# Optimization experiments

Measured on AMD Instinct MI355X. Metric: run time of the kernel, lower is better.

The kernel has to match this reference:

```python
import jax, jax.numpy as jnp
import numpy as np

NEG_SLOPE = 0.2

def gat_layer(x, src, dst, W, b, a_src, a_dst, heads, out_dim, concat):
    N = x.shape[0]
    h = (x @ W).reshape(N, heads, out_dim)            # [N,H,D]
    s_src = jnp.sum(h * a_src, axis=-1)               # [N,H]
    s_dst = jnp.sum(h * a_dst, axis=-1)               # [N,H]
    e = jax.nn.leaky_relu(s_src[src] + s_dst[dst], NEG_SLOPE)  # [E,H]
    # segment softmax over destination nodes (self-loops guarantee nonempty segments)
    m = jax.ops.segment_max(e, dst, num_segments=N)
    e = jnp.exp(e - m[dst])
    denom = jax.ops.segment_sum(e, dst, num_segments=N)
    alpha = e / denom[dst]                            # [E,H]
    msg = h[src] * alpha[:, :, None]                  # [E,H,D]
    out = jax.ops.segment_sum(msg, dst, num_segments=N)  # [N,H,D]
    if concat:
        out = out.reshape(N, heads * out_dim)
    else:
        out = out.mean(axis=1)
    return out + b

def setup_inputs() -> dict:
    key = jax.random.key(0)
    ks = jax.random.split(key, 16)
    N, E = 50000, 1600000
    IN, HID, OUT, H = 128, 256, 32, 4
    D = HID // H
    def glorot(k, shape):
        fan = shape[0] + shape[-1]
        return jax.random.uniform(k, shape, jnp.float32, -1.0, 1.0) * np.sqrt(6.0 / fan)
    x = jax.random.normal(ks[0], (N, IN), jnp.float32)
    edge_index = jax.random.randint(ks[1], (2, E), 0, N, jnp.int32)
    return {
        "x": x, "edge_index": edge_index,
        "W0": glorot(ks[2], (IN, H * D)), "b0": jnp.zeros((H * D,), jnp.float32),
        "asrc0": glorot(ks[3], (H, D)), "adst0": glorot(ks[4], (H, D)),
        "W1": glorot(ks[5], (HID, H * D)), "b1": jnp.zeros((H * D,), jnp.float32),
        "asrc1": glorot(ks[6], (H, D)), "adst1": glorot(ks[7], (H, D)),
        "W2": glorot(ks[8], (HID, 1 * OUT)), "b2": jnp.zeros((OUT,), jnp.float32),
        "asrc2": glorot(ks[9], (1, OUT)), "adst2": glorot(ks[10], (1, OUT)),
    }

def reference(x, edge_index, W0, b0, asrc0, adst0, W1, b1, asrc1, adst1, W2, b2, asrc2, adst2):
    N = x.shape[0]
    # add self-loops (PyG GATConv default)
    loop = jnp.arange(N, dtype=edge_index.dtype)
    src = jnp.concatenate([edge_index[0], loop])
    dst = jnp.concatenate([edge_index[1], loop])
    h = gat_layer(x, src, dst, W0, b0, asrc0, adst0, heads=4, out_dim=64, concat=True)
    h = jax.nn.elu(h)
    h = gat_layer(h, src, dst, W1, b1, asrc1, adst1, heads=4, out_dim=64, concat=True)
    h = jax.nn.elu(h)
    h = gat_layer(h, src, dst, W2, b2, asrc2, adst2, heads=1, out_dim=32, concat=False)
    return jax.nn.log_softmax(h, axis=1)
```

## Files before the change

### kernel.cpp

```cpp
#include <hip/hip_runtime.h>
#include <hip/hip_bf16.h>
#include <math.h>

#define IN_DIM 128
#define HID    256
#define OUTD   32
#define HEADS  4
#define NB_SH  7
#define BUCKET_CAP 6144
#define NCHUNK_BLKS 256
#define DCAP   96

typedef __attribute__((ext_vector_type(8))) short s8v;
typedef __attribute__((ext_vector_type(4))) float f4v;

__device__ inline unsigned short f2bf(float f) {
    union { __hip_bfloat16 b; unsigned short u; } cv;
    cv.b = __float2bfloat16(f);
    return cv.u;
}


__global__ __launch_bounds__(256) void csr_hist(const int* __restrict__ ei,
                                                int* __restrict__ H,
                                                int E, int N, int NB, int per_blk) {
    __shared__ int hist[512];
    int t = threadIdx.x;
    for (int i = t; i < NB; i += 256) hist[i] = 0;
    __syncthreads();
    int lo = blockIdx.x * per_blk;
    int hi = min(lo + per_blk, E + N);
    for (int e = lo + t; e < hi; e += 256) {
        int dst = (e < E) ? ei[E + e] : (e - E);
        atomicAdd(&hist[dst >> NB_SH], 1);
    }
    __syncthreads();
    for (int i = t; i < NB; i += 256) H[blockIdx.x * NB + i] = hist[i];
}

__global__ __launch_bounds__(256) void csr_colscan(int* __restrict__ H,
                                                   int* __restrict__ total, int NB) {
    int b = blockIdx.x, t = threadIdx.x;
    int v = H[t * NB + b];
    __shared__ int s[256];
    s[t] = v;
    __syncthreads();
    for (int o = 1; o < 256; o <<= 1) {
        int x = (t >= o) ? s[t - o] : 0;
        __syncthreads();
        s[t] += x;
        __syncthreads();
    }
    H[t * NB + b] = s[t] - v;
    if (t == 255) total[b] = s[255];
}

__global__ void csr_basescan(const int* __restrict__ total, int* __restrict__ base, int NB) {
    __shared__ int s[512];
    int t = threadIdx.x;
    int v = (t < NB) ? total[t] : 0;
    s[t] = v;
    __syncthreads();
    for (int o = 1; o < 512; o <<= 1) {
        int x = (t >= o) ? s[t - o] : 0;
        __syncthreads();
        s[t] += x;
        __syncthreads();
    }
    if (t < NB) base[t] = s[t] - v;
    if (t == NB - 1) base[NB] = s[t];
}

__global__ __launch_bounds__(256) void csr_partition(const int* __restrict__ ei,
                                                     const int* __restrict__ H,
                                                     const int* __restrict__ base,
                                                     int* __restrict__ ebuf,
                                                     int E, int N, int per_blk, int NB) {
    __shared__ int cur[512];
    int t = threadIdx.x;
    for (int i = t; i < NB; i += 256) cur[i] = base[i] + H[blockIdx.x * NB + i];
    __syncthreads();
    int lo = blockIdx.x * per_blk;
    int hi = min(lo + per_blk, E + N);
    for (int e = lo + t; e < hi; e += 256) {
        int src = (e < E) ? ei[e] : (e - E);
        int dst = (e < E) ? ei[E + e] : (e - E);
        int pos = atomicAdd(&cur[dst >> NB_SH], 1);
        ebuf[pos] = src | ((dst & 127) << 16);
    }
}

__global__ __launch_bounds__(256) void csr_sort(const int* __restrict__ ebuf,
                                                const int* __restrict__ base,
                                                int* __restrict__ col,
                                                int* __restrict__ rp, int N, int NB) {
    int b = blockIdx.x, t = threadIdx.x;
    int lo = base[b], hi = base[b + 1];
    int nbase = b << NB_SH;
    __shared__ int c_[128], sc[128], cur[128];
    __shared__ int loc[BUCKET_CAP];
    if (t < 128) c_[t] = 0;
    __syncthreads();
    for (int k = lo + t; k < hi; k += 256) atomicAdd(&c_[(ebuf[k] >> 16) & 127], 1);
    __syncthreads();
    if (t < 128) sc[t] = c_[t];
    __syncthreads();
    for (int o = 1; o < 128; o <<= 1) {
        int x = 0;
        if (t < 128 && t >= o) x = sc[t - o];
        __syncthreads();
        if (t < 128) sc[t] += x;
        __syncthreads();
    }
    if (t < 128) {
        int excl = sc[t] - c_[t];
        cur[t] = excl;
        int node = nbase + t;
        if (node < N) rp[node] = lo + excl;
    }
    if (b == NB - 1 && t == 0) rp[N] = hi;
    __syncthreads();
    for (int k = lo + t; k < hi; k += 256) {
        int e = ebuf[k];
        int p = atomicAdd(&cur[(e >> 16) & 127], 1);
        if (p < BUCKET_CAP) loc[p] = e & 0xFFFF;
    }
    __syncthreads();
    int m = min(hi - lo, BUCKET_CAP);
    for (int k = t; k < m; k += 256) col[lo + k] = loc[k];
}


__global__ __launch_bounds__(256) void prep_w(const float* __restrict__ W,
                                              unsigned short* __restrict__ Wt_h,
                                              unsigned short* __restrict__ Wt_l,
                                              int K, int N) {
    int idx = blockIdx.x * 256 + threadIdx.x;
    if (idx >= K * N) return;
    int n = idx / K, k = idx % K;
    float x = W[(size_t)k * N + n];
    unsigned short h = f2bf(x);
    float hf = __uint_as_float((unsigned)h << 16);
    Wt_h[idx] = h;
    Wt_l[idx] = f2bf(x - hf);
}

__global__ __launch_bounds__(256) void prep_x(const float* __restrict__ X,
                                              unsigned short* __restrict__ Xh,
                                              unsigned short* __restrict__ Xl,
                                              int total8) {
    int idx = blockIdx.x * 256 + threadIdx.x;
    if (idx >= total8) return;
    size_t b = (size_t)idx * 8;
    float4 v0 = *(const float4*)(X + b);
    float4 v1 = *(const float4*)(X + b + 4);
    float x[8] = {v0.x, v0.y, v0.z, v0.w, v1.x, v1.y, v1.z, v1.w};
    union { unsigned short s[8]; uint4 q; } h, l;
#pragma unroll
    for (int j = 0; j < 8; j++) {
        h.s[j] = f2bf(x[j]);
        l.s[j] = f2bf(x[j] - __uint_as_float((unsigned)h.s[j] << 16));
    }
    *(uint4*)(Xh + b) = h.q;
    *(uint4*)(Xl + b) = l.q;
}


template <int BN>
__global__ __launch_bounds__(256, 2) void gemm_mfma(const unsigned short* __restrict__ Ah,
                                                    const unsigned short* __restrict__ Al,
                                                    const unsigned short* __restrict__ Wt_h,
                                                    const unsigned short* __restrict__ Wt_l,
                                                    unsigned short* __restrict__ Cb,
                                                    const float* __restrict__ asrc,
                                                    const float* __restrict__ adst,
                                                    float* __restrict__ ssrcO,
                                                    float* __restrict__ sdstO,
                                                    int M, int K, int Nst, int Hn) {
    constexpr int WROWS = (BN == 128) ? 64 : 32;
    constexpr int WCOLS = (BN == 128) ? 64 : 32;
    constexpr int MI = WROWS / 16, NJ = WCOLS / 16;
    __shared__ unsigned short As_h[128][64], As_l[128][64];
    __shared__ unsigned short Bs_h[BN][64], Bs_l[BN][64];
    int tid = threadIdx.x;
    int lane = tid & 63, w = tid >> 6;
    int wm, wn;
    if (BN == 128) { wm = w & 1; wn = w >> 1; } else { wm = w; wn = 0; }
    int row0 = blockIdx.x * 128, col0 = blockIdx.y * BN;

    f4v acc[MI][NJ];
#pragma unroll
    for (int i = 0; i < MI; i++)
#pragma unroll
        for (int j = 0; j < NJ; j++) acc[i][j] = (f4v)(0.f);

    for (int k0 = 0; k0 < K; k0 += 64) {
#pragma unroll
        for (int i = 0; i < 4; i++) {
            int cidx = tid + i * 256;
            int r = cidx >> 3, ch = cidx & 7;
            int grow = row0 + r;
            uint4 vh = make_uint4(0, 0, 0, 0), vl = make_uint4(0, 0, 0, 0);
            if (grow < M) {
                size_t g = (size_t)grow * K + k0 + ch * 8;
                vh = *(const uint4*)(Ah + g);
                vl = *(const uint4*)(Al + g);
            }
            int chs = ch ^ (r & 7);
            *(uint4*)&As_h[r][chs * 8] = vh;
            *(uint4*)&As_l[r][chs * 8] = vl;
        }
#pragma unroll
        for (int i = 0; i < BN * 8 / 256; i++) {
            int cidx = tid + i * 256;
            int n = cidx >> 3, ch = cidx & 7;
            int chs = ch ^ (n & 7);
            size_t g = (size_t)(col0 + n) * K + k0 + ch * 8;
            *(uint4*)&Bs_h[n][chs * 8] = *(const uint4*)(Wt_h + g);
            *(uint4*)&Bs_l[n][chs * 8] = *(const uint4*)(Wt_l + g);
        }
        __syncthreads();
#pragma unroll
        for (int ks = 0; ks < 2; ks++) {
            s8v ah[MI], al[MI], bh[NJ], bl[NJ];
            int kc = ks * 4 + (lane >> 4);
            int lr = lane & 15;
#pragma unroll
            for (int i = 0; i < MI; i++) {
                int r = wm * WROWS + i * 16 + lr;
                ah[i] = *(const s8v*)&As_h[r][(kc ^ (r & 7)) * 8];
                al[i] = *(const s8v*)&As_l[r][(kc ^ (r & 7)) * 8];
            }
#pragma unroll
            for (int j = 0; j < NJ; j++) {
                int n = wn * WCOLS + j * 16 + lr;
                bh[j] = *(const s8v*)&Bs_h[n][(kc ^ (n & 7)) * 8];
                bl[j] = *(const s8v*)&Bs_l[n][(kc ^ (n & 7)) * 8];
            }
#pragma unroll
            for (int i = 0; i < MI; i++)
#pragma unroll
                for (int j = 0; j < NJ; j++) {
                    acc[i][j] = __builtin_amdgcn_mfma_f32_16x16x32_bf16(ah[i], bh[j], acc[i][j], 0, 0, 0);
                    acc[i][j] = __builtin_amdgcn_mfma_f32_16x16x32_bf16(ah[i], bl[j], acc[i][j], 0, 0, 0);
                    acc[i][j] = __builtin_amdgcn_mfma_f32_16x16x32_bf16(al[i], bh[j], acc[i][j], 0, 0, 0);
                }
        }
        __syncthreads();
    }
    int lr = lane & 15, lg = lane >> 4;
#pragma unroll
    for (int i = 0; i < MI; i++)
#pragma unroll
        for (int j = 0; j < NJ; j++) {
            int gcol = col0 + wn * WCOLS + j * 16 + lr;
#pragma unroll
            for (int rr = 0; rr < 4; rr++) {
                int grow = row0 + wm * WROWS + i * 16 + lg * 4 + rr;
                if (grow < M) Cb[(size_t)grow * Nst + gcol] = f2bf(acc[i][j][rr]);
            }
        }
    int hd = (BN == 128) ? (blockIdx.y * 2 + wn) : 0;
    float as_[NJ], ad_[NJ];
#pragma unroll
    for (int j = 0; j < NJ; j++) {
        int gcol = col0 + wn * WCOLS + j * 16 + lr;
        as_[j] = asrc[gcol];
        ad_[j] = adst[gcol];
    }
#pragma unroll
    for (int i = 0; i < MI; i++)
#pragma unroll
        for (int rr = 0; rr < 4; rr++) {
            float ps = 0.f, pd = 0.f;
#pragma unroll
            for (int j = 0; j < NJ; j++) {
                ps += acc[i][j][rr] * as_[j];
                pd += acc[i][j][rr] * ad_[j];
            }
#pragma unroll
            for (int off = 1; off < 16; off <<= 1) {
                ps += __shfl_xor(ps, off);
                pd += __shfl_xor(pd, off);
            }
            int grow = row0 + wm * WROWS + i * 16 + lg * 4 + rr;
            if (lr == 0 && grow < M) {
                ssrcO[(size_t)grow * Hn + hd] = ps;
                sdstO[(size_t)grow * Hn + hd] = pd;
            }
        }
}


__global__ __launch_bounds__(256) void gat_fused256(const unsigned short* __restrict__ hb,
                                                    const float* __restrict__ ssrc,
                                                    const float* __restrict__ sdst,
                                                    const int* __restrict__ rp,
                                                    const int* __restrict__ col,
                                                    const float* __restrict__ bias,
                                                    unsigned short* __restrict__ outH,
                                                    unsigned short* __restrict__ outL, int N) {
    __shared__ float als[4][DCAP * 4];
    int wv = threadIdx.x >> 6, lane = threadIdx.x & 63;
    int n = blockIdx.x * 4 + wv;
    if (n >= N) return;
    int k0 = __builtin_amdgcn_readfirstlane(rp[n]);
    int k1 = __builtin_amdgcn_readfirstlane(rp[n + 1]);
    int deg = k1 - k0;

    int h1 = lane & 3, slot = lane >> 2;
    float sd1 = sdst[(size_t)n * 4 + h1];
    float m = -1e30f, l = 0.f;
    for (int k = k0 + slot; k < k1; k += 16) {
        int s = col[k];
        float e = ssrc[(size_t)s * 4 + h1] + sd1;
        e = (e > 0.f) ? e : 0.2f * e;
        float mn = fmaxf(m, e);
        l = l * __expf(m - mn) + __expf(e - mn);
        m = mn;
    }
#pragma unroll
    for (int off = 4; off < 64; off <<= 1) {
        float m2 = __shfl_xor(m, off), l2 = __shfl_xor(l, off);
        float mn = fmaxf(m, m2);
        l = l * __expf(m - mn) + l2 * __expf(m2 - mn);
        m = mn;
    }
    float invl = 1.f / l;
    bool fast = (deg <= DCAP);
    if (fast) {
        for (int k = k0 + slot; k < k1; k += 16) {
            int s = col[k];
            float e = ssrc[(size_t)s * 4 + h1] + sd1;
            e = (e > 0.f) ? e : 0.2f * e;
            als[wv][(k - k0) * 4 + h1] = __expf(e - m) * invl;
        }
    }

    int eo = lane >> 4;
    int cl = (lane & 15) * 8;
#pragma unroll
    for (int half = 0; half < 2; half++) {
        int c = half * 128 + cl;
        int head = c >> 6;
        float acc[8];
#pragma unroll
        for (int j = 0; j < 8; j++) acc[j] = 0.f;
        if (fast) {
            for (int k = k0; k < k1; k += 8) {
                int ka = k + eo, kb = k + 4 + eo;
                bool va = ka < k1, vb = kb < k1;
                int sa = col[va ? ka : k0], sb = col[vb ? kb : k0];
                int ia = va ? (ka - k0) : 0, ib = vb ? (kb - k0) : 0;
                float aa = va ? als[wv][ia * 4 + head] : 0.f;
                float ab = vb ? als[wv][ib * 4 + head] : 0.f;
                uint4 ha = *(const uint4*)(hb + (size_t)sa * 256 + c);
                uint4 hc = *(const uint4*)(hb + (size_t)sb * 256 + c);
                const unsigned* pa = (const unsigned*)&ha;
                const unsigned* pb = (const unsigned*)&hc;
#pragma unroll
                for (int q = 0; q < 4; q++) {
                    acc[2 * q]     += aa * __uint_as_float(pa[q] << 16)
                                    + ab * __uint_as_float(pb[q] << 16);
                    acc[2 * q + 1] += aa * __uint_as_float(pa[q] & 0xffff0000u)
                                    + ab * __uint_as_float(pb[q] & 0xffff0000u);
                }
            }
        } else {
            float mh = __shfl(m, head);
            float ivh = __shfl(invl, head);
            float sdh = __shfl(sd1, head);
            for (int k = k0; k < k1; k += 8) {
                int ka = k + eo, kb = k + 4 + eo;
                bool va = ka < k1, vb = kb < k1;
                int sa = col[va ? ka : k0], sb = col[vb ? kb : k0];
                float ea = ssrc[(size_t)sa * 4 + head] + sdh;
                ea = (ea > 0.f) ? ea : 0.2f * ea;
                float aa = va ? __expf(ea - mh) * ivh : 0.f;
                float eb = ssrc[(size_t)sb * 4 + head] + sdh;
                eb = (eb > 0.f) ? eb : 0.2f * eb;
                float ab = vb ? __expf(eb - mh) * ivh : 0.f;
                uint4 ha = *(const uint4*)(hb + (size_t)sa * 256 + c);
                uint4 hc = *(const uint4*)(hb + (size_t)sb * 256 + c);
                const unsigned* pa = (const unsigned*)&ha;
                const unsigned* pb = (const unsigned*)&hc;
#pragma unroll
                for (int q = 0; q < 4; q++) {
                    acc[2 * q]     += aa * __uint_as_float(pa[q] << 16)
                                    + ab * __uint_as_float(pb[q] << 16);
                    acc[2 * q + 1] += aa * __uint_as_float(pa[q] & 0xffff0000u)
                                    + ab * __uint_as_float(pb[q] & 0xffff0000u);
                }
            }
        }
#pragma unroll
        for (int off = 16; off < 64; off <<= 1)
#pragma unroll
            for (int j = 0; j < 8; j++) acc[j] += __shfl_xor(acc[j], off);
        if (eo == 0) {
            union { unsigned short s[8]; uint4 q; } ph, pl;
#pragma unroll
            for (int j = 0; j < 8; j++) {
                float v = acc[j] + bias[c + j];
                v = (v > 0.f) ? v : expm1f(v);
                ph.s[j] = f2bf(v);
                pl.s[j] = f2bf(v - __uint_as_float((unsigned)ph.s[j] << 16));
            }
            *(uint4*)(outH + (size_t)n * 256 + c) = ph.q;
            *(uint4*)(outL + (size_t)n * 256 + c) = pl.q;
        }
    }
}


__global__ __launch_bounds__(256) void gat_fused32(const unsigned short* __restrict__ hb,
                                                   const float* __restrict__ ssrc,
                                                   const float* __restrict__ sdst,
                                                   const int* __restrict__ rp,
                                                   const int* __restrict__ col,
                                                   const float* __restrict__ bias,
                                                   float* __restrict__ outF, int N) {
    const int TPE = 4, EPW = 16;
    int wv = threadIdx.x >> 6, lane = threadIdx.x & 63;
    int n = blockIdx.x * 4 + wv;
    if (n >= N) return;
    int k0 = __builtin_amdgcn_readfirstlane(rp[n]);
    int k1 = __builtin_amdgcn_readfirstlane(rp[n + 1]);

    float sd1 = sdst[n];
    float m = -1e30f, l = 0.f;
    for (int k = k0 + lane; k < k1; k += 64) {
        int s = col[k];
        float e = ssrc[s] + sd1;
        e = (e > 0.f) ? e : 0.2f * e;
        float mn = fmaxf(m, e);
        l = l * __expf(m - mn) + __expf(e - mn);
        m = mn;
    }
#pragma unroll
    for (int off = 1; off < 64; off <<= 1) {
        float m2 = __shfl_xor(m, off), l2 = __shfl_xor(l, off);
        float mn = fmaxf(m, m2);
        l = l * __expf(m - mn) + l2 * __expf(m2 - mn);
        m = mn;
    }
    float invl = 1.f / l;

    int eo = lane / TPE;
    int c = (lane % TPE) * 8;
    float acc[8];
#pragma unroll
    for (int j = 0; j < 8; j++) acc[j] = 0.f;
    for (int k = k0; k < k1; k += 2 * EPW) {
        int ka = k + eo, kb = k + EPW + eo;
        bool va = ka < k1, vb = kb < k1;
        int sa = col[va ? ka : k0], sb = col[vb ? kb : k0];
        float ea = ssrc[sa] + sd1;
        ea = (ea > 0.f) ? ea : 0.2f * ea;
        float aa = va ? __expf(ea - m) * invl : 0.f;
        float eb = ssrc[sb] + sd1;
        eb = (eb > 0.f) ? eb : 0.2f * eb;
        float ab = vb ? __expf(eb - m) * invl : 0.f;
        uint4 ha = *(const uint4*)(hb + (size_t)sa * 32 + c);
        uint4 hc = *(const uint4*)(hb + (size_t)sb * 32 + c);
        const unsigned* pa = (const unsigned*)&ha;
        const unsigned* pb = (const unsigned*)&hc;
#pragma unroll
        for (int q = 0; q < 4; q++) {
            acc[2 * q]     += aa * __uint_as_float(pa[q] << 16)
                            + ab * __uint_as_float(pb[q] << 16);
            acc[2 * q + 1] += aa * __uint_as_float(pa[q] & 0xffff0000u)
                            + ab * __uint_as_float(pb[q] & 0xffff0000u);
        }
    }
#pragma unroll
    for (int off = TPE; off < 64; off <<= 1)
#pragma unroll
        for (int j = 0; j < 8; j++) acc[j] += __shfl_xor(acc[j], off);

    float o[8];
#pragma unroll
    for (int j = 0; j < 8; j++) o[j] = acc[j] + bias[c + j];
    float mx = o[0];
#pragma unroll
    for (int j = 1; j < 8; j++) mx = fmaxf(mx, o[j]);
#pragma unroll
    for (int off = 1; off < TPE; off <<= 1) mx = fmaxf(mx, __shfl_xor(mx, off));
    float sm = 0.f;
#pragma unroll
    for (int j = 0; j < 8; j++) sm += __expf(o[j] - mx);
#pragma unroll
    for (int off = 1; off < TPE; off <<= 1) sm += __shfl_xor(sm, off);
    float lg = logf(sm) + mx;
    if (eo != 0) return;
    float4* op = (float4*)(outF + (size_t)n * 32 + c);
    op[0] = make_float4(o[0] - lg, o[1] - lg, o[2] - lg, o[3] - lg);
    op[1] = make_float4(o[4] - lg, o[5] - lg, o[6] - lg, o[7] - lg);
}


extern "C" void kernel_launch(void* const* d_in, const int* in_sizes, int n_in,
                              void* d_out, int out_size, void* d_ws, size_t ws_size,
                              hipStream_t stream) {
    const float* x   = (const float*)d_in[0];
    const int*   ei  = (const int*)d_in[1];
    const float* W0  = (const float*)d_in[2];
    const float* b0  = (const float*)d_in[3];
    const float* as0 = (const float*)d_in[4];
    const float* ad0 = (const float*)d_in[5];
    const float* W1  = (const float*)d_in[6];
    const float* b1  = (const float*)d_in[7];
    const float* as1 = (const float*)d_in[8];
    const float* ad1 = (const float*)d_in[9];
    const float* W2  = (const float*)d_in[10];
    const float* b2  = (const float*)d_in[11];
    const float* as2 = (const float*)d_in[12];
    const float* ad2 = (const float*)d_in[13];

    int N = in_sizes[0] / IN_DIM;
    int E = in_sizes[1] / 2;
    int Et = E + N;
    int NB = (N + 127) >> NB_SH;

    char* w = (char*)d_ws;
    size_t off = 0;
    auto alloc = [&](size_t bytes) -> void* {
        void* p = w + off;
        off = (off + bytes + 255) & ~(size_t)255;
        return p;
    };
    unsigned short* Qh    = (unsigned short*)alloc((size_t)N * HID * 2);
    unsigned short* Ql    = (unsigned short*)alloc((size_t)N * HID * 2);
    unsigned short* Ab    = (unsigned short*)alloc((size_t)N * HID * 2);
    unsigned short* xh    = (unsigned short*)alloc((size_t)N * IN_DIM * 2);
    unsigned short* xl    = (unsigned short*)alloc((size_t)N * IN_DIM * 2);
    float*          ssrc  = (float*)alloc((size_t)N * HEADS * 4);
    float*          sdst  = (float*)alloc((size_t)N * HEADS * 4);
    int*            rp    = (int*)alloc((size_t)(N + 1) * 4);
    int*            col   = (int*)alloc((size_t)Et * 4);
    int*            H     = (int*)alloc((size_t)NCHUNK_BLKS * NB * 4);
    int*            total = (int*)alloc((size_t)(NB + 1) * 4);
    int*            base  = (int*)alloc((size_t)(NB + 1) * 4);
    int*            ebuf  = (int*)alloc((size_t)Et * 4);
    unsigned short* Wt0h  = (unsigned short*)alloc((size_t)IN_DIM * HID * 2);
    unsigned short* Wt0l  = (unsigned short*)alloc((size_t)IN_DIM * HID * 2);
    unsigned short* Wt1h  = (unsigned short*)alloc((size_t)HID * HID * 2);
    unsigned short* Wt1l  = (unsigned short*)alloc((size_t)HID * HID * 2);
    unsigned short* Wt2h  = (unsigned short*)alloc((size_t)HID * OUTD * 2);
    unsigned short* Wt2l  = (unsigned short*)alloc((size_t)HID * OUTD * 2);

    prep_w<<<(IN_DIM * HID + 255) / 256, 256, 0, stream>>>(W0, Wt0h, Wt0l, IN_DIM, HID);
    prep_w<<<(HID * HID + 255) / 256, 256, 0, stream>>>(W1, Wt1h, Wt1l, HID, HID);
    prep_w<<<(HID * OUTD + 255) / 256, 256, 0, stream>>>(W2, Wt2h, Wt2l, HID, OUTD);
    int t8 = N * IN_DIM / 8;
    prep_x<<<(t8 + 255) / 256, 256, 0, stream>>>(x, xh, xl, t8);

    int per_blk = (Et + NCHUNK_BLKS - 1) / NCHUNK_BLKS;
    csr_hist<<<NCHUNK_BLKS, 256, 0, stream>>>(ei, H, E, N, NB, per_blk);
    csr_colscan<<<NB, 256, 0, stream>>>(H, total, NB);
    csr_basescan<<<1, 512, 0, stream>>>(total, base, NB);
    csr_partition<<<NCHUNK_BLKS, 256, 0, stream>>>(ei, H, base, ebuf, E, N, per_blk, NB);
    csr_sort<<<NB, 256, 0, stream>>>(ebuf, base, col, rp, N, NB);

    dim3 gm((N + 127) / 128, 2);
    dim3 gm2((N + 127) / 128, 1);
    int gg = (N + 3) / 4;

    gemm_mfma<128><<<gm, 256, 0, stream>>>(xh, xl, Wt0h, Wt0l, Ab, as0, ad0, ssrc, sdst,
                                           N, IN_DIM, HID, HEADS);
    gat_fused256<<<gg, 256, 0, stream>>>(Ab, ssrc, sdst, rp, col, b0, Qh, Ql, N);

    gemm_mfma<128><<<gm, 256, 0, stream>>>(Qh, Ql, Wt1h, Wt1l, Ab, as1, ad1, ssrc, sdst,
                                           N, HID, HID, HEADS);
    gat_fused256<<<gg, 256, 0, stream>>>(Ab, ssrc, sdst, rp, col, b1, Qh, Ql, N);

    gemm_mfma<32><<<gm2, 256, 0, stream>>>(Qh, Ql, Wt2h, Wt2l, Ab, as2, ad2, ssrc, sdst,
                                           N, HID, OUTD, 1);
    gat_fused32<<<gg, 256, 0, stream>>>(Ab, ssrc, sdst, rp, col, b2, (float*)d_out, N);
}
```

Before: 470.3 us.

## Split GAT aggregation into per-slice gathers with precomputed packed edge alphas

The GEMM now writes its 256-wide output in a slice-major layout of 32-column slices. A separate edge_alpha kernel computes the softmax coefficients once per edge and head, packing a 16-bit source index with an fp16 alpha. Eight gather_slice launches then aggregate one 3.2 MB slice at a time, so the random source-row gathers can stay within an L2-sized working set. The cost is rereading the packed edge list eight times per layer. The change also adds fp16 rounding of alpha and a 16-bit node index that only holds while N is below 65536.

```diff
diff --git a/kernel.cpp b/kernel.cpp
--- a/kernel.cpp
+++ b/kernel.cpp
@@ -1,5 +1,6 @@
 #include <hip/hip_runtime.h>
 #include <hip/hip_bf16.h>
+#include <hip/hip_fp16.h>
 #include <math.h>
 
 #define IN_DIM 128
@@ -9,7 +10,6 @@
 #define NB_SH  7
 #define BUCKET_CAP 6144
 #define NCHUNK_BLKS 256
-#define DCAP   96
 
 typedef __attribute__((ext_vector_type(8))) short s8v;
 typedef __attribute__((ext_vector_type(4))) float f4v;
@@ -257,7 +257,14 @@
 #pragma unroll
             for (int rr = 0; rr < 4; rr++) {
                 int grow = row0 + wm * WROWS + i * 16 + lg * 4 + rr;
-                if (grow < M) Cb[(size_t)grow * Nst + gcol] = f2bf(acc[i][j][rr]);
+                if (grow < M) {
+                    if (BN == 128) {
+                        Cb[((size_t)(gcol >> 5) * M + grow) * 32 + (gcol & 31)] =
+                            f2bf(acc[i][j][rr]);
+                    } else {
+                        Cb[(size_t)grow * Nst + gcol] = f2bf(acc[i][j][rr]);
+                    }
+                }
             }
         }
     int hd = (BN == 128) ? (blockIdx.y * 2 + wn) : 0;
@@ -292,22 +299,17 @@
 }
 
 
-__global__ __launch_bounds__(256) void gat_fused256(const unsigned short* __restrict__ hb,
-                                                    const float* __restrict__ ssrc,
-                                                    const float* __restrict__ sdst,
-                                                    const int* __restrict__ rp,
-                                                    const int* __restrict__ col,
-                                                    const float* __restrict__ bias,
-                                                    unsigned short* __restrict__ outH,
-                                                    unsigned short* __restrict__ outL, int N) {
-    __shared__ float als[4][DCAP * 4];
+__global__ __launch_bounds__(256) void edge_alpha(const float* __restrict__ ssrc,
+                                                  const float* __restrict__ sdst,
+                                                  const int* __restrict__ rp,
+                                                  const int* __restrict__ col,
+                                                  unsigned* __restrict__ colA,
+                                                  int N, int Et) {
     int wv = threadIdx.x >> 6, lane = threadIdx.x & 63;
     int n = blockIdx.x * 4 + wv;
     if (n >= N) return;
     int k0 = __builtin_amdgcn_readfirstlane(rp[n]);
     int k1 = __builtin_amdgcn_readfirstlane(rp[n + 1]);
-    int deg = k1 - k0;
-
     int h1 = lane & 3, slot = lane >> 2;
     float sd1 = sdst[(size_t)n * 4 + h1];
     float m = -1e30f, l = 0.f;
@@ -327,89 +329,69 @@
         m = mn;
     }
     float invl = 1.f / l;
-    bool fast = (deg <= DCAP);
-    if (fast) {
-        for (int k = k0 + slot; k < k1; k += 16) {
-            int s = col[k];
-            float e = ssrc[(size_t)s * 4 + h1] + sd1;
-            e = (e > 0.f) ? e : 0.2f * e;
-            als[wv][(k - k0) * 4 + h1] = __expf(e - m) * invl;
-        }
-    }
-
-    int eo = lane >> 4;
-    int cl = (lane & 15) * 8;
-#pragma unroll
-    for (int half = 0; half < 2; half++) {
-        int c = half * 128 + cl;
-        int head = c >> 6;
-        float acc[8];
-#pragma unroll
-        for (int j = 0; j < 8; j++) acc[j] = 0.f;
-        if (fast) {
-            for (int k = k0; k < k1; k += 8) {
-                int ka = k + eo, kb = k + 4 + eo;
-                bool va = ka < k1, vb = kb < k1;
-                int sa = col[va ? ka : k0], sb = col[vb ? kb : k0];
-                int ia = va ? (ka - k0) : 0, ib = vb ? (kb - k0) : 0;
-                float aa = va ? als[wv][ia * 4 + head] : 0.f;
-                float ab = vb ? als[wv][ib * 4 + head] : 0.f;
-                uint4 ha = *(const uint4*)(hb + (size_t)sa * 256 + c);
-                uint4 hc = *(const uint4*)(hb + (size_t)sb * 256 + c);
-                const unsigned* pa = (const unsigned*)&ha;
-                const unsigned* pb = (const unsigned*)&hc;
-#pragma unroll
-                for (int q = 0; q < 4; q++) {
-                    acc[2 * q]     += aa * __uint_as_float(pa[q] << 16)
-                                    + ab * __uint_as_float(pb[q] << 16);
-                    acc[2 * q + 1] += aa * __uint_as_float(pa[q] & 0xffff0000u)
-                                    + ab * __uint_as_float(pb[q] & 0xffff0000u);
-                }
-            }
-        } else {
-            float mh = __shfl(m, head);
-            float ivh = __shfl(invl, head);
-            float sdh = __shfl(sd1, head);
-            for (int k = k0; k < k1; k += 8) {
-                int ka = k + eo, kb = k + 4 + eo;
-                bool va = ka < k1, vb = kb < k1;
-                int sa = col[va ? ka : k0], sb = col[vb ? kb : k0];
-                float ea = ssrc[(size_t)sa * 4 + head] + sdh;
-                ea = (ea > 0.f) ? ea : 0.2f * ea;
-                float aa = va ? __expf(ea - mh) * ivh : 0.f;
-                float eb = ssrc[(size_t)sb * 4 + head] + sdh;
-                eb = (eb > 0.f) ? eb : 0.2f * eb;
-                float ab = vb ? __expf(eb - mh) * ivh : 0.f;
-                uint4 ha = *(const uint4*)(hb + (size_t)sa * 256 + c);
-                uint4 hc = *(const uint4*)(hb + (size_t)sb * 256 + c);
-                const unsigned* pa = (const unsigned*)&ha;
-                const unsigned* pb = (const unsigned*)&hc;
-#pragma unroll
-                for (int q = 0; q < 4; q++) {
-                    acc[2 * q]     += aa * __uint_as_float(pa[q] << 16)
-                                    + ab * __uint_as_float(pb[q] << 16);
-                    acc[2 * q + 1] += aa * __uint_as_float(pa[q] & 0xffff0000u)
-                                    + ab * __uint_as_float(pb[q] & 0xffff0000u);
-                }
-            }
-        }
-#pragma unroll
-        for (int off = 16; off < 64; off <<= 1)
-#pragma unroll
-            for (int j = 0; j < 8; j++) acc[j] += __shfl_xor(acc[j], off);
-        if (eo == 0) {
-            union { unsigned short s[8]; uint4 q; } ph, pl;
-#pragma unroll
-            for (int j = 0; j < 8; j++) {
-                float v = acc[j] + bias[c + j];
-                v = (v > 0.f) ? v : expm1f(v);
-                ph.s[j] = f2bf(v);
-                pl.s[j] = f2bf(v - __uint_as_float((unsigned)ph.s[j] << 16));
-            }
-            *(uint4*)(outH + (size_t)n * 256 + c) = ph.q;
-            *(uint4*)(outL + (size_t)n * 256 + c) = pl.q;
-        }
-    }
+    for (int k = k0 + slot; k < k1; k += 16) {
+        int s = col[k];
+        float e = ssrc[(size_t)s * 4 + h1] + sd1;
+        e = (e > 0.f) ? e : 0.2f * e;
+        float a = __expf(e - m) * invl;
+        unsigned short au = __half_as_ushort(__float2half(a));
+        colA[(size_t)h1 * Et + k] = (unsigned)s | ((unsigned)au << 16);
+    }
+}
+
+
+__global__ __launch_bounds__(256) void gather_slice(const unsigned short* __restrict__ hsp,
+                                                    const unsigned* __restrict__ colAh,
+                                                    const int* __restrict__ rp,
+                                                    const float* __restrict__ bias,
+                                                    unsigned short* __restrict__ outH,
+                                                    unsigned short* __restrict__ outL,
+                                                    int N, int p) {
+    int wv = threadIdx.x >> 6, lane = threadIdx.x & 63;
+    int n = blockIdx.x * 4 + wv;
+    if (n >= N) return;
+    int k0 = __builtin_amdgcn_readfirstlane(rp[n]);
+    int k1 = __builtin_amdgcn_readfirstlane(rp[n + 1]);
+    int eo = lane >> 2;
+    int cl = (lane & 3) * 8;
+    float acc[8];
+#pragma unroll
+    for (int j = 0; j < 8; j++) acc[j] = 0.f;
+    for (int k = k0; k < k1; k += 32) {
+        int ka = k + eo, kb = k + 16 + eo;
+        bool va = ka < k1, vb = kb < k1;
+        unsigned wa = colAh[va ? ka : k0];
+        unsigned wb = colAh[vb ? kb : k0];
+        float aa = va ? __half2float(__ushort_as_half((unsigned short)(wa >> 16))) : 0.f;
+        float ab = vb ? __half2float(__ushort_as_half((unsigned short)(wb >> 16))) : 0.f;
+        uint4 ha = *(const uint4*)(hsp + (size_t)(wa & 0xFFFF) * 32 + cl);
+        uint4 hc = *(const uint4*)(hsp + (size_t)(wb & 0xFFFF) * 32 + cl);
+        const unsigned* pa = (const unsigned*)&ha;
+        const unsigned* pb = (const unsigned*)&hc;
+#pragma unroll
+        for (int q = 0; q < 4; q++) {
+            acc[2 * q]     += aa * __uint_as_float(pa[q] << 16)
+                            + ab * __uint_as_float(pb[q] << 16);
+            acc[2 * q + 1] += aa * __uint_as_float(pa[q] & 0xffff0000u)
+                            + ab * __uint_as_float(pb[q] & 0xffff0000u);
+        }
+    }
+#pragma unroll
+    for (int off = 4; off < 64; off <<= 1)
+#pragma unroll
+        for (int j = 0; j < 8; j++) acc[j] += __shfl_xor(acc[j], off);
+    if (eo != 0) return;
+    int c = p * 32 + cl;
+    union { unsigned short s[8]; uint4 q; } ph, pl;
+#pragma unroll
+    for (int j = 0; j < 8; j++) {
+        float v = acc[j] + bias[c + j];
+        v = (v > 0.f) ? v : expm1f(v);
+        ph.s[j] = f2bf(v);
+        pl.s[j] = f2bf(v - __uint_as_float((unsigned)ph.s[j] << 16));
+    }
+    *(uint4*)(outH + (size_t)n * 256 + c) = ph.q;
+    *(uint4*)(outL + (size_t)n * 256 + c) = pl.q;
 }
 
 
@@ -538,6 +520,7 @@
     float*          sdst  = (float*)alloc((size_t)N * HEADS * 4);
     int*            rp    = (int*)alloc((size_t)(N + 1) * 4);
     int*            col   = (int*)alloc((size_t)Et * 4);
+    unsigned*       colA  = (unsigned*)alloc((size_t)HEADS * Et * 4);
     int*            H     = (int*)alloc((size_t)NCHUNK_BLKS * NB * 4);
     int*            total = (int*)alloc((size_t)(NB + 1) * 4);
     int*            base  = (int*)alloc((size_t)(NB + 1) * 4);
@@ -568,11 +551,19 @@
 
     gemm_mfma<128><<<gm, 256, 0, stream>>>(xh, xl, Wt0h, Wt0l, Ab, as0, ad0, ssrc, sdst,
                                            N, IN_DIM, HID, HEADS);
-    gat_fused256<<<gg, 256, 0, stream>>>(Ab, ssrc, sdst, rp, col, b0, Qh, Ql, N);
+    edge_alpha<<<gg, 256, 0, stream>>>(ssrc, sdst, rp, col, colA, N, Et);
+    for (int p = 0; p < 8; p++)
+        gather_slice<<<gg, 256, 0, stream>>>(Ab + (size_t)p * N * 32,
+                                             colA + (size_t)(p >> 1) * Et,
+                                             rp, b0, Qh, Ql, N, p);
 
     gemm_mfma<128><<<gm, 256, 0, stream>>>(Qh, Ql, Wt1h, Wt1l, Ab, as1, ad1, ssrc, sdst,
                                            N, HID, HID, HEADS);
-    gat_fused256<<<gg, 256, 0, stream>>>(Ab, ssrc, sdst, rp, col, b1, Qh, Ql, N);
+    edge_alpha<<<gg, 256, 0, stream>>>(ssrc, sdst, rp, col, colA, N, Et);
+    for (int p = 0; p < 8; p++)
+        gather_slice<<<gg, 256, 0, stream>>>(Ab + (size_t)p * N * 32,
+                                             colA + (size_t)(p >> 1) * Et,
+                                             rp, b1, Qh, Ql, N, p);
 
     gemm_mfma<32><<<gm2, 256, 0, stream>>>(Qh, Ql, Wt2h, Wt2l, Ab, as2, ad2, ssrc, sdst,
                                            N, HID, OUTD, 1);
```

New measurement: 811.0 us. 1.72x slower.
